# Kernel optimization log

Measured on AMD Instinct MI355X. Metric: run time of the kernel, lower is better.

Reference implementation:

```python
import jax, jax.numpy as jnp
import numpy as np

B, S, D = 16, 2048, 128
SCALE = 1.0 / float(np.sqrt(D))  # scale = 1/sqrt(dim_K) per docstring


def setup_inputs() -> dict:
    key = jax.random.key(0)
    kq, kk, kv = jax.random.split(key, 3)
    Q = jax.random.normal(kq, (B, S, D), dtype=jnp.float32)
    K = jax.random.normal(kk, (B, S, D), dtype=jnp.float32)
    V = jax.random.normal(kv, (B, S, D), dtype=jnp.float32)
    return {"Q": Q, "K": K, "V": V}


def reference(Q, K, V):
    # attention = Q @ K^T * scale  -> [B, S, S]
    attn = jnp.einsum('bqd,bkd->bqk', Q, K) * SCALE
    attn = jax.nn.softmax(attn, axis=-1)
    # context = attn @ V -> [B, S, D]
    context = jnp.einsum('bqk,bkd->bqd', attn, V)
    return context
```

## Files before the change

### kernel.cpp

```cpp
#include <hip/hip_runtime.h>
#include <hip/hip_bf16.h>


#define NB 16
#define NS 2048
#define ND 128
#define KVBLK 64
#define NT (NS / KVBLK)
#define NHT (NT / 2)
#define IMGB 32768
#define QSC (0.08838834764831845f * 1.4426950408889634f)

typedef __attribute__((ext_vector_type(8))) short bf16x8;
typedef __attribute__((ext_vector_type(4))) short short4v;
typedef __attribute__((ext_vector_type(16))) float f32x16;
typedef __attribute__((ext_vector_type(4))) int int4v;

__device__ __forceinline__ short f2bf(float f) {
    unsigned u = __builtin_bit_cast(unsigned, f);
    return (short)((u + 0x7fffu + ((u >> 16) & 1u)) >> 16);
}

#if __has_builtin(__builtin_amdgcn_exp2f)
#define EXP2F(x) __builtin_amdgcn_exp2f(x)
#else
#define EXP2F(x) __expf((x) * 0.6931471805599453f)
#endif

__device__ __forceinline__ void gll16(const void* g, void* l) {
    __builtin_amdgcn_global_load_lds(
        (const __attribute__((address_space(1))) uint32_t*)g,
        (__attribute__((address_space(3))) uint32_t*)l, 16, 0, 0);
}

__global__ __launch_bounds__(256, 2)
void prep_kv(const float* __restrict__ Kg, const float* __restrict__ Vg,
             uint8_t* __restrict__ ws) {
    __shared__ __align__(16) uint8_t img[IMGB];
    const int tid = threadIdx.x;
    const int t = blockIdx.x, b = blockIdx.y;
    const float* Kb = Kg + ((size_t)b * NS + (size_t)t * KVBLK) * ND;
    const float* Vb = Vg + ((size_t)b * NS + (size_t)t * KVBLK) * ND;
#pragma unroll
    for (int it = 0; it < 8; ++it) {
        int idx = it * 256 + tid;
        int r  = idx >> 5;
        int c4 = (idx & 31) << 2;
        float4 kvv = *(const float4*)(Kb + (size_t)r * ND + c4);
        short4v ks = { f2bf(kvv.x), f2bf(kvv.y), f2bf(kvv.z), f2bf(kvv.w) };
        *(short4v*)&img[r * 256 + ((c4 * 2) ^ ((r & 7) << 4))] = ks;
        float4 vv = *(const float4*)(Vb + (size_t)r * ND + c4);
        float vf[4] = { vv.x, vv.y, vv.z, vv.w };
#pragma unroll
        for (int di = 0; di < 4; ++di) {
            int d = c4 + di;
            *(short*)&img[16384 + d * 128 + ((r * 2) ^ ((d & 7) << 4))] = f2bf(vf[di]);
        }
    }
    __syncthreads();
    float4* dst = (float4*)(ws + (size_t)(b * NT + t) * IMGB);
    const float4* srcl = (const float4*)img;
#pragma unroll
    for (int j = 0; j < 8; ++j)
        dst[j * 256 + tid] = srcl[j * 256 + tid];
}

__global__ __launch_bounds__(512, 2)
void sdpa_fwd(const float* __restrict__ Qg, const uint8_t* __restrict__ ws,
              float* __restrict__ Og) {
    __shared__ __align__(16) uint8_t kv[2][2][IMGB];

    const int tid  = threadIdx.x;
    const int w    = tid >> 6;
    const int wq   = w & 3;
    const int wh   = w >> 2;
    const int lane = tid & 63;
    const int lr_  = lane & 31;
    const int hi   = lane >> 5;
    const int xr   = (lane & 7) << 4;

    const int gid  = blockIdx.x;
    const int b    = (gid & 7) * 2 + ((gid >> 3) & 1);
    const int qblk = gid >> 4;
    const int q0w  = qblk * 128 + wq * 32;

    bf16x8 qf[8];
    {
        const float* qrow = Qg + ((size_t)b * NS + q0w + lr_) * ND;
#pragma unroll
        for (int dc = 0; dc < 8; ++dc) {
            const float4* p = (const float4*)(qrow + dc * 16 + hi * 8);
            float4 x0 = p[0], x1 = p[1];
            bf16x8 f;
            f[0] = f2bf(x0.x * QSC); f[1] = f2bf(x0.y * QSC);
            f[2] = f2bf(x0.z * QSC); f[3] = f2bf(x0.w * QSC);
            f[4] = f2bf(x1.x * QSC); f[5] = f2bf(x1.y * QSC);
            f[6] = f2bf(x1.z * QSC); f[7] = f2bf(x1.w * QSC);
            qf[dc] = f;
        }
    }

    f32x16 acc[4];
#pragma unroll
    for (int n = 0; n < 4; ++n)
#pragma unroll
        for (int r = 0; r < 16; ++r) acc[n][r] = 0.f;
    float l_run = 0.f;

    const uint8_t* wsb = ws + (size_t)b * NT * IMGB;

    auto stage = [&](int bfi, int it) {
        const uint8_t* src = wsb + (size_t)(wh * NHT + it) * IMGB
                                 + (size_t)(wq * 8192 + lane * 16);
        uint8_t* dst = &kv[bfi][wh][wq * 8192];
#pragma unroll
        for (int i = 0; i < 8; ++i)
            gll16(src + i * 1024, dst + i * 1024);
    };

    const int kbase = lr_ * 256 + ((hi * 16) ^ xr);
    const int vbase = 16384 + lr_ * 128 + ((hi * 16) ^ xr);

    int buf = 0;
    stage(0, 0);
    __syncthreads();

    for (int t = 0; t < NHT; ++t) {
        if (t + 1 < NHT) stage(buf ^ 1, t + 1);

        const uint8_t* img = kv[buf][wh];

        f32x16 s0a, s0b, s1a, s1b;
#pragma unroll
        for (int r = 0; r < 16; ++r) { s0a[r] = 0.f; s0b[r] = 0.f;
                                       s1a[r] = 0.f; s1b[r] = 0.f; }
        __builtin_amdgcn_s_setprio(1);
#pragma unroll
        for (int dc = 0; dc < 4; ++dc) {
            const uint8_t* ka = img + (kbase ^ ((2 * dc) * 32));
            const uint8_t* kb2 = img + (kbase ^ ((2 * dc + 1) * 32));
            bf16x8 k0 = *(const bf16x8*)ka;
            bf16x8 k1 = *(const bf16x8*)(ka + 8192);
            bf16x8 k2 = *(const bf16x8*)kb2;
            bf16x8 k3 = *(const bf16x8*)(kb2 + 8192);
            s0a = __builtin_amdgcn_mfma_f32_32x32x16_bf16(k0, qf[2*dc],   s0a, 0, 0, 0);
            s1a = __builtin_amdgcn_mfma_f32_32x32x16_bf16(k1, qf[2*dc],   s1a, 0, 0, 0);
            s0b = __builtin_amdgcn_mfma_f32_32x32x16_bf16(k2, qf[2*dc+1], s0b, 0, 0, 0);
            s1b = __builtin_amdgcn_mfma_f32_32x32x16_bf16(k3, qf[2*dc+1], s1b, 0, 0, 0);
        }
        __builtin_amdgcn_s_setprio(0);

        f32x16 s0 = s0a + s0b;
        f32x16 s1 = s1a + s1b;
#pragma unroll
        for (int r = 0; r < 16; ++r) {
            s0[r] = EXP2F(s0[r]);
            s1[r] = EXP2F(s1[r]);
        }
        float u8[8];
#pragma unroll
        for (int i = 0; i < 8; ++i)
            u8[i] = (s0[2*i] + s0[2*i+1]) + (s1[2*i] + s1[2*i+1]);
        l_run += ((u8[0] + u8[1]) + (u8[2] + u8[3]))
               + ((u8[4] + u8[5]) + (u8[6] + u8[7]));

        int W[16];
#define PK(dst, x, y) asm("v_cvt_pk_bf16_f32 %0, %1, %2" : "=v"(dst) : "v"(x), "v"(y))
        PK(W[0],  s0[0],  s0[1]);  PK(W[1],  s0[2],  s0[3]);
        PK(W[2],  s0[4],  s0[5]);  PK(W[3],  s0[6],  s0[7]);
        PK(W[4],  s0[8],  s0[9]);  PK(W[5],  s0[10], s0[11]);
        PK(W[6],  s0[12], s0[13]); PK(W[7],  s0[14], s0[15]);
        PK(W[8],  s1[0],  s1[1]);  PK(W[9],  s1[2],  s1[3]);
        PK(W[10], s1[4],  s1[5]);  PK(W[11], s1[6],  s1[7]);
        PK(W[12], s1[8],  s1[9]);  PK(W[13], s1[10], s1[11]);
        PK(W[14], s1[12], s1[13]); PK(W[15], s1[14], s1[15]);
#undef PK
        bf16x8 pa[4];
#pragma unroll
        for (int g = 0; g < 4; ++g) {
            int a0 = W[g * 4 + 0], b0 = W[g * 4 + 2];
            int a1 = W[g * 4 + 1], b1 = W[g * 4 + 3];
            asm("v_permlane32_swap_b32 %0, %1" : "+v"(a0), "+v"(b0));
            asm("v_permlane32_swap_b32 %0, %1" : "+v"(a1), "+v"(b1));
            int4v A = { a0, a1, b0, b1 };
            pa[g] = __builtin_bit_cast(bf16x8, A);
        }

        __builtin_amdgcn_s_setprio(1);
#pragma unroll
        for (int n = 0; n < 4; ++n) {
#pragma unroll
            for (int kc = 0; kc < 4; ++kc) {
                bf16x8 vf = *(const bf16x8*)(img + ((vbase ^ (kc * 32)) + n * 4096));
                acc[n] = __builtin_amdgcn_mfma_f32_32x32x16_bf16(pa[kc], vf, acc[n], 0, 0, 0);
            }
        }
        __builtin_amdgcn_s_setprio(0);

        __syncthreads();
        buf ^= 1;
    }

    l_run += __shfl_xor(l_run, 32);

    float* scr = (float*)&kv[0][0][0];
    const int sbase = wq * 4224 + lane * 66;
    if (wh == 1) {
#pragma unroll
        for (int n = 0; n < 4; ++n)
#pragma unroll
            for (int r = 0; r < 16; ++r) scr[sbase + n * 16 + r] = acc[n][r];
        scr[sbase + 64] = l_run;
    }
    __syncthreads();
    if (wh == 0) {
        float lc = l_run + scr[sbase + 64];
        float li[16];
#pragma unroll
        for (int r = 0; r < 16; ++r)
            li[r] = 1.f / __shfl(lc, (r & 3) + 8 * (r >> 2) + 4 * hi);
        float* ob = Og + ((size_t)b * NS + q0w) * ND + lr_;
#pragma unroll
        for (int r = 0; r < 16; ++r) {
            int row = (r & 3) + 8 * (r >> 2) + 4 * hi;
#pragma unroll
            for (int n = 0; n < 4; ++n)
                ob[(size_t)row * ND + n * 32] =
                    (acc[n][r] + scr[sbase + n * 16 + r]) * li[r];
        }
    }
}

extern "C" void kernel_launch(void* const* d_in, const int* in_sizes, int n_in,
                              void* d_out, int out_size, void* d_ws, size_t ws_size,
                              hipStream_t stream) {
    const float* Q = (const float*)d_in[0];
    const float* K = (const float*)d_in[1];
    const float* V = (const float*)d_in[2];
    float* O = (float*)d_out;
    (void)in_sizes; (void)n_in; (void)out_size; (void)ws_size;
    uint8_t* ws = (uint8_t*)d_ws;
    prep_kv<<<dim3(NT, NB), 256, 0, stream>>>(K, V, ws);
    sdpa_fwd<<<dim3(NB * NS / 128, 1), 512, 0, stream>>>(Q, ws, O);
}
```

Measured before the change: 57.60 us.

## Read K/V images directly from global memory instead of LDS staging

Removes the double-buffered LDS staging of K/V tiles via global_load_lds and has each wave load its MFMA operands straight from the global workspace. The XOR swizzle is dropped from both the prep kernel layout and the consumer addressing, and the V transpose now writes byte-by-byte. This eliminates the per-iteration barrier and the LDS footprint, which could raise occupancy, but it replaces LDS reads with redundant global/L2 reads shared across waves and loses load-compute overlap.

```diff
diff --git a/kernel.cpp b/kernel.cpp
--- a/kernel.cpp
+++ b/kernel.cpp
@@ -27,12 +27,6 @@
 #define EXP2F(x) __expf((x) * 0.6931471805599453f)
 #endif
 
-__device__ __forceinline__ void gll16(const void* g, void* l) {
-    __builtin_amdgcn_global_load_lds(
-        (const __attribute__((address_space(1))) uint32_t*)g,
-        (__attribute__((address_space(3))) uint32_t*)l, 16, 0, 0);
-}
-
 __global__ __launch_bounds__(256, 2)
 void prep_kv(const float* __restrict__ Kg, const float* __restrict__ Vg,
              uint8_t* __restrict__ ws) {
@@ -48,13 +42,14 @@
         int c4 = (idx & 31) << 2;
         float4 kvv = *(const float4*)(Kb + (size_t)r * ND + c4);
         short4v ks = { f2bf(kvv.x), f2bf(kvv.y), f2bf(kvv.z), f2bf(kvv.w) };
-        *(short4v*)&img[r * 256 + ((c4 * 2) ^ ((r & 7) << 4))] = ks;
+        *(short4v*)&img[r * 256 + c4 * 2] = ks;
         float4 vv = *(const float4*)(Vb + (size_t)r * ND + c4);
         float vf[4] = { vv.x, vv.y, vv.z, vv.w };
 #pragma unroll
         for (int di = 0; di < 4; ++di) {
             int d = c4 + di;
-            *(short*)&img[16384 + d * 128 + ((r * 2) ^ ((d & 7) << 4))] = f2bf(vf[di]);
+            img[16384 + d * 128 + r * 2]     = (uint8_t)(f2bf(vf[di]) & 0xff);
+            img[16384 + d * 128 + r * 2 + 1] = (uint8_t)((f2bf(vf[di]) >> 8) & 0xff);
         }
     }
     __syncthreads();
@@ -68,7 +63,7 @@
 __global__ __launch_bounds__(512, 2)
 void sdpa_fwd(const float* __restrict__ Qg, const uint8_t* __restrict__ ws,
               float* __restrict__ Og) {
-    __shared__ __align__(16) uint8_t kv[2][2][IMGB];
+    __shared__ float scr[4][64][66];
 
     const int tid  = threadIdx.x;
     const int w    = tid >> 6;
@@ -77,7 +72,6 @@
     const int lane = tid & 63;
     const int lr_  = lane & 31;
     const int hi   = lane >> 5;
-    const int xr   = (lane & 7) << 4;
 
     const int gid  = blockIdx.x;
     const int b    = (gid & 7) * 2 + ((gid >> 3) & 1);
@@ -107,28 +101,13 @@
         for (int r = 0; r < 16; ++r) acc[n][r] = 0.f;
     float l_run = 0.f;
 
-    const uint8_t* wsb = ws + (size_t)b * NT * IMGB;
-
-    auto stage = [&](int bfi, int it) {
-        const uint8_t* src = wsb + (size_t)(wh * NHT + it) * IMGB
-                                 + (size_t)(wq * 8192 + lane * 16);
-        uint8_t* dst = &kv[bfi][wh][wq * 8192];
-#pragma unroll
-        for (int i = 0; i < 8; ++i)
-            gll16(src + i * 1024, dst + i * 1024);
-    };
-
-    const int kbase = lr_ * 256 + ((hi * 16) ^ xr);
-    const int vbase = 16384 + lr_ * 128 + ((hi * 16) ^ xr);
-
-    int buf = 0;
-    stage(0, 0);
-    __syncthreads();
+    const int kbase = lr_ * 256 + hi * 16;
+    const int vbase = 16384 + lr_ * 128 + hi * 16;
+    const uint8_t* img0 = ws + (size_t)b * NT * IMGB
+                             + (size_t)(wh * NHT) * IMGB;
 
     for (int t = 0; t < NHT; ++t) {
-        if (t + 1 < NHT) stage(buf ^ 1, t + 1);
-
-        const uint8_t* img = kv[buf][wh];
+        const uint8_t* img = img0 + (size_t)t * IMGB;
 
         f32x16 s0a, s0b, s1a, s1b;
 #pragma unroll
@@ -137,8 +116,8 @@
         __builtin_amdgcn_s_setprio(1);
 #pragma unroll
         for (int dc = 0; dc < 4; ++dc) {
-            const uint8_t* ka = img + (kbase ^ ((2 * dc) * 32));
-            const uint8_t* kb2 = img + (kbase ^ ((2 * dc + 1) * 32));
+            const uint8_t* ka  = img + kbase + (2 * dc) * 32;
+            const uint8_t* kb2 = img + kbase + (2 * dc + 1) * 32;
             bf16x8 k0 = *(const bf16x8*)ka;
             bf16x8 k1 = *(const bf16x8*)(ka + 8192);
             bf16x8 k2 = *(const bf16x8*)kb2;
@@ -191,30 +170,25 @@
         for (int n = 0; n < 4; ++n) {
 #pragma unroll
             for (int kc = 0; kc < 4; ++kc) {
-                bf16x8 vf = *(const bf16x8*)(img + ((vbase ^ (kc * 32)) + n * 4096));
+                bf16x8 vf = *(const bf16x8*)(img + vbase + kc * 32 + n * 4096);
                 acc[n] = __builtin_amdgcn_mfma_f32_32x32x16_bf16(pa[kc], vf, acc[n], 0, 0, 0);
             }
         }
         __builtin_amdgcn_s_setprio(0);
-
-        __syncthreads();
-        buf ^= 1;
     }
 
     l_run += __shfl_xor(l_run, 32);
 
-    float* scr = (float*)&kv[0][0][0];
-    const int sbase = wq * 4224 + lane * 66;
     if (wh == 1) {
 #pragma unroll
         for (int n = 0; n < 4; ++n)
 #pragma unroll
-            for (int r = 0; r < 16; ++r) scr[sbase + n * 16 + r] = acc[n][r];
-        scr[sbase + 64] = l_run;
+            for (int r = 0; r < 16; ++r) scr[wq][lane][n * 16 + r] = acc[n][r];
+        scr[wq][lane][64] = l_run;
     }
     __syncthreads();
     if (wh == 0) {
-        float lc = l_run + scr[sbase + 64];
+        float lc = l_run + scr[wq][lane][64];
         float li[16];
 #pragma unroll
         for (int r = 0; r < 16; ++r)
@@ -226,7 +200,7 @@
 #pragma unroll
             for (int n = 0; n < 4; ++n)
                 ob[(size_t)row * ND + n * 32] =
-                    (acc[n][r] + scr[sbase + n * 16 + r]) * li[r];
+                    (acc[n][r] + scr[wq][lane][n * 16 + r]) * li[r];
         }
     }
 }
```

After: 137.6 us. +138.8%, slower.
